# Kernel tuning notes

Hardware: AMD Instinct MI355X
Metric: run time of the kernel (lower is better)

## Reference

```python
import jax, jax.numpy as jnp
import numpy as np

B, T, D, H = 8, 512, 1024, 16
DH = D // H  # per-head feature dim (64)


def setup_inputs() -> dict:
    key = jax.random.key(0)
    ks = jax.random.split(key, 10)
    s = 1.0 / np.sqrt(DH)
    inp = {
        "X_data": jax.random.normal(ks[0], (B, T, D), dtype=jnp.float32),
        "mask": jnp.ones((B, T), dtype=jnp.int32),
        # per-head Q/K/V projections (each SelfAttention has its own d_h x d_h weights)
        "Wq": jax.random.normal(ks[1], (H, DH, DH), dtype=jnp.float32) * s,
        "bq": jnp.zeros((H, DH), dtype=jnp.float32),
        "Wk": jax.random.normal(ks[2], (H, DH, DH), dtype=jnp.float32) * s,
        "bk": jnp.zeros((H, DH), dtype=jnp.float32),
        "Wv": jax.random.normal(ks[3], (H, DH, DH), dtype=jnp.float32) * s,
        "bv": jnp.zeros((H, DH), dtype=jnp.float32),
        # AttentionFusion: linear on concatenated head outputs -> len_feature_new
        "Wf": jax.random.normal(ks[4], (D, D), dtype=jnp.float32) * (1.0 / np.sqrt(D)),
        "bf": jnp.zeros((D,), dtype=jnp.float32),
    }
    return inp


def reference(X_data, mask, Wq, bq, Wk, bk, Wv, bv, Wf, bf):
    # Split features into heads: [B, T, H, DH] (equal partitions since D % H == 0)
    Xh = X_data.reshape(B, T, H, DH)
    # Batched per-head projections (replaces the Python loop over heads)
    Q = jnp.einsum("bthd,hde->bhte", Xh, Wq) + bq[None, :, None, :]
    K = jnp.einsum("bthd,hde->bhte", Xh, Wk) + bk[None, :, None, :]
    V = jnp.einsum("bthd,hde->bhte", Xh, Wv) + bv[None, :, None, :]
    scale = 1.0 / jnp.sqrt(jnp.asarray(DH, dtype=Q.dtype))
    scores = jnp.einsum("bhqe,bhke->bhqk", Q, K) * scale  # [B, H, T, T]
    scores = jnp.where(mask[:, None, None, :] > 0, scores, jnp.asarray(-1e9, scores.dtype))
    att = jax.nn.softmax(scores, axis=-1)
    out = jnp.einsum("bhqk,bhke->bhqe", att, V)  # [B, H, T, DH]
    # Concatenate heads (same order as the per-head loop) and fuse
    out = out.transpose(0, 2, 1, 3).reshape(B, T, D)
    fused = out @ Wf + bf  # AttentionFusion linear
    return fused
```

## Files before the change

### kernel.cpp

```cpp
#include <hip/hip_runtime.h>
#include <math.h>

#define B 8
#define T 512
#define D 1024
#define H 16
#define DH 64

typedef __bf16 bf16;
typedef __attribute__((ext_vector_type(8))) __bf16 bf16x8;
typedef __attribute__((ext_vector_type(4))) __bf16 bf16x4;
typedef __attribute__((ext_vector_type(4))) float f32x4;

__device__ __forceinline__ void gld16(const void* g, void* l) {
    __builtin_amdgcn_global_load_lds(
        (const __attribute__((address_space(1))) void*)g,
        (__attribute__((address_space(3))) void*)l, 16, 0, 0);
}


__global__ __launch_bounds__(256) void wft_kernel(
    const float* __restrict__ Wf, bf16* __restrict__ WfT)
{
    __shared__ bf16 Ts[64 * 72];
    const int k0 = (blockIdx.x >> 4) * 64;
    const int n0 = (blockIdx.x & 15) * 64;
    const int tid = threadIdx.x;
    for (int i = tid; i < 1024; i += 256) {
        const int k = i >> 4, nq = (i & 15) * 4;
        const float4 w = *(const float4*)(Wf + (size_t)(k0 + k) * D + n0 + nq);
        Ts[(nq + 0) * 72 + k] = (bf16)w.x;
        Ts[(nq + 1) * 72 + k] = (bf16)w.y;
        Ts[(nq + 2) * 72 + k] = (bf16)w.z;
        Ts[(nq + 3) * 72 + k] = (bf16)w.w;
    }
    __syncthreads();
    for (int i = tid; i < 512; i += 256) {
        const int n = i >> 3, kc = (i & 7) * 8;
        *(bf16x8*)(WfT + (size_t)(n0 + n) * D + k0 + kc) = *(const bf16x8*)&Ts[n * 72 + kc];
    }
}

__global__ __launch_bounds__(256) void qkv_mfma(
    const float* __restrict__ X,
    const float* __restrict__ Wq, const float* __restrict__ bq,
    const float* __restrict__ Wk, const float* __restrict__ bk,
    const float* __restrict__ Wv, const float* __restrict__ bv,
    bf16* __restrict__ Qb, bf16* __restrict__ Kb, bf16* __restrict__ Vtb)
{
    __shared__ bf16 As[128 * 72];
    __shared__ bf16 Bq[64 * 72];
    __shared__ bf16 Bk[64 * 72];
    __shared__ bf16 Bv[64 * 72];
    __shared__ bf16 Vt_l[64 * 136];

    const int bh = blockIdx.x >> 2;
    const int t0 = (blockIdx.x & 3) * 128;
    const int b = bh >> 4, h = bh & 15;
    const int tid = threadIdx.x;
    const int wave = tid >> 6, lane = tid & 63;
    const int quad = lane >> 4, l15 = lane & 15;

    for (int i = tid; i < 2048; i += 256) {
        const int row = i >> 4, cq = (i & 15) * 4;
        const float4 x = *(const float4*)(X + ((size_t)b * T + t0 + row) * D + h * DH + cq);
        bf16x4 t;
        t[0] = (bf16)x.x; t[1] = (bf16)x.y; t[2] = (bf16)x.z; t[3] = (bf16)x.w;
        *(bf16x4*)&As[row * 72 + cq] = t;
    }
    for (int i = tid; i < 1024; i += 256) {
        const int d = i >> 4, eq = (i & 15) * 4;
        const float4 wq4 = *(const float4*)(Wq + h * 4096 + d * 64 + eq);
        const float4 wk4 = *(const float4*)(Wk + h * 4096 + d * 64 + eq);
        const float4 wv4 = *(const float4*)(Wv + h * 4096 + d * 64 + eq);
        Bq[(eq + 0) * 72 + d] = (bf16)wq4.x; Bq[(eq + 1) * 72 + d] = (bf16)wq4.y;
        Bq[(eq + 2) * 72 + d] = (bf16)wq4.z; Bq[(eq + 3) * 72 + d] = (bf16)wq4.w;
        Bk[(eq + 0) * 72 + d] = (bf16)wk4.x; Bk[(eq + 1) * 72 + d] = (bf16)wk4.y;
        Bk[(eq + 2) * 72 + d] = (bf16)wk4.z; Bk[(eq + 3) * 72 + d] = (bf16)wk4.w;
        Bv[(eq + 0) * 72 + d] = (bf16)wv4.x; Bv[(eq + 1) * 72 + d] = (bf16)wv4.y;
        Bv[(eq + 2) * 72 + d] = (bf16)wv4.z; Bv[(eq + 3) * 72 + d] = (bf16)wv4.w;
    }
    __syncthreads();

    bf16x8 af[2][2];
#pragma unroll
    for (int mt = 0; mt < 2; ++mt)
#pragma unroll
        for (int ks = 0; ks < 2; ++ks)
            af[mt][ks] = *(const bf16x8*)&As[(wave * 32 + mt * 16 + l15) * 72 + ks * 32 + quad * 8];

    auto compute = [&](const bf16* Bmat, f32x4 acc[2][4]) {
#pragma unroll
        for (int ks = 0; ks < 2; ++ks) {
            bf16x8 bfr[4];
#pragma unroll
            for (int nt = 0; nt < 4; ++nt)
                bfr[nt] = *(const bf16x8*)&Bmat[(nt * 16 + l15) * 72 + ks * 32 + quad * 8];
#pragma unroll
            for (int mt = 0; mt < 2; ++mt)
#pragma unroll
                for (int nt = 0; nt < 4; ++nt)
                    acc[mt][nt] = __builtin_amdgcn_mfma_f32_16x16x32_bf16(
                        af[mt][ks], bfr[nt], acc[mt][nt], 0, 0, 0);
        }
    };

    const size_t bhTD = (size_t)bh * T * DH;

    {
        f32x4 acc[2][4] = {};
        compute(Bq, acc);
#pragma unroll
        for (int mt = 0; mt < 2; ++mt)
#pragma unroll
            for (int nt = 0; nt < 4; ++nt) {
                const int e = nt * 16 + l15;
                const float bias = bq[h * DH + e];
#pragma unroll
                for (int reg = 0; reg < 4; ++reg) {
                    const int t = t0 + wave * 32 + mt * 16 + quad * 4 + reg;
                    Qb[bhTD + (size_t)t * DH + e] = (bf16)((acc[mt][nt][reg] + bias) * 0.125f);
                }
            }
    }
    {
        f32x4 acc[2][4] = {};
        compute(Bk, acc);
#pragma unroll
        for (int mt = 0; mt < 2; ++mt)
#pragma unroll
            for (int nt = 0; nt < 4; ++nt) {
                const int e = nt * 16 + l15;
                const float bias = bk[h * DH + e];
#pragma unroll
                for (int reg = 0; reg < 4; ++reg) {
                    const int t = t0 + wave * 32 + mt * 16 + quad * 4 + reg;
                    Kb[bhTD + (size_t)t * DH + e] = (bf16)(acc[mt][nt][reg] + bias);
                }
            }
    }
    {
        f32x4 acc[2][4] = {};
        compute(Bv, acc);
#pragma unroll
        for (int mt = 0; mt < 2; ++mt)
#pragma unroll
            for (int nt = 0; nt < 4; ++nt) {
                const int e = nt * 16 + l15;
                const float bias = bv[h * DH + e];
#pragma unroll
                for (int reg = 0; reg < 4; ++reg) {
                    const int tl = wave * 32 + mt * 16 + quad * 4 + reg;
                    Vt_l[e * 136 + tl] = (bf16)(acc[mt][nt][reg] + bias);
                }
            }
    }
    __syncthreads();
    for (int i = tid; i < 1024; i += 256) {
        const int e = i >> 4, c = (i & 15) * 8;
        const bf16x8 t = *(const bf16x8*)&Vt_l[e * 136 + c];
        *(bf16x8*)(Vtb + (size_t)bh * DH * T + (size_t)e * T + t0 + c) = t;
    }
}

__global__ __launch_bounds__(256) void attn_mfma(
    const bf16* __restrict__ Qb, const bf16* __restrict__ Kb,
    const bf16* __restrict__ Vtb, const int* __restrict__ mask,
    bf16* __restrict__ Ob)
{
    __shared__ bf16 Ks[64 * 64];
    __shared__ bf16 Vts[64 * 64];
    __shared__ bf16 Pl[4][32 * 72];
    __shared__ int ms[64];

    const int bh = blockIdx.x >> 2;
    const int q0 = (blockIdx.x & 3) * 128;
    const int b = bh >> 4, h = bh & 15;
    const int tid = threadIdx.x;
    const int wave = tid >> 6, lane = tid & 63;
    const int quad = lane >> 4, l15 = lane & 15;
    const int lrow = lane >> 3, lcol8 = (lane & 7) * 8;

    const size_t bhTD = (size_t)bh * T * DH;
    const size_t bhDT = (size_t)bh * DH * T;

    bf16x8 qf[2][2];
#pragma unroll
    for (int mt = 0; mt < 2; ++mt)
#pragma unroll
        for (int ks = 0; ks < 2; ++ks)
            qf[mt][ks] = *(const bf16x8*)(Qb + bhTD +
                (size_t)(q0 + wave * 32 + mt * 16 + l15) * DH + ks * 32 + quad * 8);

    f32x4 acc[2][4] = {};
    float lst[2][4] = {};

    for (int kt = 0; kt < 8; ++kt) {
        const int k0 = kt * 64;
        __syncthreads();
        {
            const int r0 = wave * 16;
            gld16(Kb + bhTD + (size_t)(k0 + r0 + lrow) * DH + lcol8, &Ks[r0 * 64]);
            gld16(Kb + bhTD + (size_t)(k0 + r0 + 8 + lrow) * DH + lcol8, &Ks[(r0 + 8) * 64]);
            gld16(Vtb + bhDT + (size_t)(r0 + lrow) * T + k0 + lcol8, &Vts[r0 * 64]);
            gld16(Vtb + bhDT + (size_t)(r0 + 8 + lrow) * T + k0 + lcol8, &Vts[(r0 + 8) * 64]);
            if (tid < 64) ms[tid] = mask[(size_t)b * T + k0 + tid];
        }
        __syncthreads();

        bf16x8 kf[4][2];
#pragma unroll
        for (int nt = 0; nt < 4; ++nt)
#pragma unroll
            for (int ks = 0; ks < 2; ++ks)
                kf[nt][ks] = *(const bf16x8*)&Ks[(nt * 16 + l15) * 64 + ks * 32 + quad * 8];
        int mv[4];
#pragma unroll
        for (int nt = 0; nt < 4; ++nt) mv[nt] = ms[nt * 16 + l15];

#pragma unroll
        for (int mt = 0; mt < 2; ++mt) {
            f32x4 s[4] = {};
#pragma unroll
            for (int ks = 0; ks < 2; ++ks)
#pragma unroll
                for (int nt = 0; nt < 4; ++nt)
                    s[nt] = __builtin_amdgcn_mfma_f32_16x16x32_bf16(qf[mt][ks], kf[nt][ks], s[nt], 0, 0, 0);
#pragma unroll
            for (int nt = 0; nt < 4; ++nt)
#pragma unroll
                for (int reg = 0; reg < 4; ++reg) {
                    const float p = (mv[nt] > 0) ? __expf(s[nt][reg]) : 0.f;
                    lst[mt][reg] += p;
                    Pl[wave][(mt * 16 + quad * 4 + reg) * 72 + nt * 16 + l15] = (bf16)p;
                }
        }
        __builtin_amdgcn_wave_barrier();

        bf16x8 vf[4][2];
#pragma unroll
        for (int nt = 0; nt < 4; ++nt)
#pragma unroll
            for (int kc = 0; kc < 2; ++kc)
                vf[nt][kc] = *(const bf16x8*)&Vts[(nt * 16 + l15) * 64 + kc * 32 + quad * 8];
#pragma unroll
        for (int mt = 0; mt < 2; ++mt) {
            bf16x8 pf[2];
#pragma unroll
            for (int kc = 0; kc < 2; ++kc)
                pf[kc] = *(const bf16x8*)&Pl[wave][(mt * 16 + l15) * 72 + kc * 32 + quad * 8];
#pragma unroll
            for (int nt = 0; nt < 4; ++nt)
#pragma unroll
                for (int kc = 0; kc < 2; ++kc)
                    acc[mt][nt] = __builtin_amdgcn_mfma_f32_16x16x32_bf16(pf[kc], vf[nt][kc], acc[mt][nt], 0, 0, 0);
        }
    }

#pragma unroll
    for (int mt = 0; mt < 2; ++mt)
#pragma unroll
        for (int reg = 0; reg < 4; ++reg) {
            float l = lst[mt][reg];
            l += __shfl_xor(l, 1);
            l += __shfl_xor(l, 2);
            l += __shfl_xor(l, 4);
            l += __shfl_xor(l, 8);
            const float inv = 1.f / l;
            const int t = q0 + wave * 32 + mt * 16 + quad * 4 + reg;
#pragma unroll
            for (int nt = 0; nt < 4; ++nt)
                Ob[((size_t)b * T + t) * D + h * DH + nt * 16 + l15] =
                    (bf16)(acc[mt][nt][reg] * inv);
        }
}

__global__ __launch_bounds__(256) void fuse_mfma(
    const bf16* __restrict__ Ob, const bf16* __restrict__ WfT,
    const float* __restrict__ bfv, float* __restrict__ out)
{
    __shared__ bf16 As[128 * 64];
    __shared__ bf16 Bs[128 * 64];

    const int col0 = blockIdx.x * 128;
    const int row0 = blockIdx.y * 128;
    const int tid = threadIdx.x;
    const int wave = tid >> 6, lane = tid & 63;
    const int quad = lane >> 4, l15 = lane & 15;
    const int lrow = lane >> 3, lcol8 = (lane & 7) * 8;
    const int wm = (wave >> 1) * 64, wn = (wave & 1) * 64;

    f32x4 acc[4][4] = {};

    for (int k0 = 0; k0 < D; k0 += 64) {
        __syncthreads();
        const int r0 = wave * 32;
#pragma unroll
        for (int j = 0; j < 4; ++j) {
            gld16(Ob + (size_t)(row0 + r0 + j * 8 + lrow) * D + k0 + lcol8, &As[(r0 + j * 8) * 64]);
            gld16(WfT + (size_t)(col0 + r0 + j * 8 + lrow) * D + k0 + lcol8, &Bs[(r0 + j * 8) * 64]);
        }
        __syncthreads();
#pragma unroll
        for (int ks = 0; ks < 2; ++ks) {
            bf16x8 af[4], bfr[4];
#pragma unroll
            for (int mt = 0; mt < 4; ++mt)
                af[mt] = *(const bf16x8*)&As[(wm + mt * 16 + l15) * 64 + ks * 32 + quad * 8];
#pragma unroll
            for (int nt = 0; nt < 4; ++nt)
                bfr[nt] = *(const bf16x8*)&Bs[(wn + nt * 16 + l15) * 64 + ks * 32 + quad * 8];
#pragma unroll
            for (int mt = 0; mt < 4; ++mt)
#pragma unroll
                for (int nt = 0; nt < 4; ++nt)
                    acc[mt][nt] = __builtin_amdgcn_mfma_f32_16x16x32_bf16(af[mt], bfr[nt], acc[mt][nt], 0, 0, 0);
        }
    }

    float bias[4];
#pragma unroll
    for (int nt = 0; nt < 4; ++nt) bias[nt] = bfv[col0 + wn + nt * 16 + l15];
#pragma unroll
    for (int mt = 0; mt < 4; ++mt)
#pragma unroll
        for (int reg = 0; reg < 4; ++reg) {
            const int r = row0 + wm + mt * 16 + quad * 4 + reg;
#pragma unroll
            for (int nt = 0; nt < 4; ++nt)
                out[(size_t)r * D + col0 + wn + nt * 16 + l15] = acc[mt][nt][reg] + bias[nt];
        }
}

extern "C" void kernel_launch(void* const* d_in, const int* in_sizes, int n_in,
                              void* d_out, int out_size, void* d_ws, size_t ws_size,
                              hipStream_t stream) {
    const float* X   = (const float*)d_in[0];
    const int* mask  = (const int*)d_in[1];
    const float* Wq  = (const float*)d_in[2];
    const float* bq  = (const float*)d_in[3];
    const float* Wk  = (const float*)d_in[4];
    const float* bk  = (const float*)d_in[5];
    const float* Wv  = (const float*)d_in[6];
    const float* bv  = (const float*)d_in[7];
    const float* Wf  = (const float*)d_in[8];
    const float* bfv = (const float*)d_in[9];
    float* out = (float*)d_out;

    bf16* wsb = (bf16*)d_ws;
    const size_t QN = (size_t)B * H * T * DH;
    bf16* Qb  = wsb;
    bf16* Kb  = wsb + QN;
    bf16* Vtb = wsb + 2 * QN;
    bf16* Ob  = wsb + 3 * QN;
    bf16* WfT = wsb + 4 * QN;

    wft_kernel<<<dim3(256), 256, 0, stream>>>(Wf, WfT);
    qkv_mfma<<<dim3(B * H * 4), 256, 0, stream>>>(X, Wq, bq, Wk, bk, Wv, bv, Qb, Kb, Vtb);
    attn_mfma<<<dim3(B * H * 4), 256, 0, stream>>>(Qb, Kb, Vtb, mask, Ob);
    fuse_mfma<<<dim3(D / 128, (B * T) / 128), 256, 0, stream>>>(Ob, WfT, bfv, out);
}
```

Baseline: 148.3 us.

## Add prep kernel for bf16 casts, XOR-swizzle LDS, enlarge attention key tiles, shrink fuse tiles

A single prep kernel now converts X to bf16 and transposes the per-head Wq/Wk/Wv and Wf weights into bf16, so qkv_mfma can stage its operands with global_load_lds and XOR-swizzled LDS layouts. Attention processes 128-key tiles instead of 64, halving the K/V loop iterations and barriers, and uses swizzled K/Vt tiles. The fuse GEMM drops to 128x64 tiles, doubling the block count for occupancy. In exchange it adds an extra pass over X through memory and uses more LDS in attention.

```diff
diff --git a/kernel.cpp b/kernel.cpp
--- a/kernel.cpp
+++ b/kernel.cpp
@@ -19,66 +19,88 @@
 }
 
 
-__global__ __launch_bounds__(256) void wft_kernel(
-    const float* __restrict__ Wf, bf16* __restrict__ WfT)
+__global__ __launch_bounds__(256) void prep_kernel(
+    const float* __restrict__ X,
+    const float* __restrict__ Wq, const float* __restrict__ Wk,
+    const float* __restrict__ Wv, const float* __restrict__ Wf,
+    bf16* __restrict__ Xb, bf16* __restrict__ WqT, bf16* __restrict__ WkT,
+    bf16* __restrict__ WvT, bf16* __restrict__ WfT)
 {
     __shared__ bf16 Ts[64 * 72];
-    const int k0 = (blockIdx.x >> 4) * 64;
-    const int n0 = (blockIdx.x & 15) * 64;
-    const int tid = threadIdx.x;
-    for (int i = tid; i < 1024; i += 256) {
-        const int k = i >> 4, nq = (i & 15) * 4;
-        const float4 w = *(const float4*)(Wf + (size_t)(k0 + k) * D + n0 + nq);
-        Ts[(nq + 0) * 72 + k] = (bf16)w.x;
-        Ts[(nq + 1) * 72 + k] = (bf16)w.y;
-        Ts[(nq + 2) * 72 + k] = (bf16)w.z;
-        Ts[(nq + 3) * 72 + k] = (bf16)w.w;
-    }
-    __syncthreads();
-    for (int i = tid; i < 512; i += 256) {
-        const int n = i >> 3, kc = (i & 7) * 8;
-        *(bf16x8*)(WfT + (size_t)(n0 + n) * D + k0 + kc) = *(const bf16x8*)&Ts[n * 72 + kc];
+    const int blk = blockIdx.x, tid = threadIdx.x;
+    if (blk < 256) {
+        const float4* src = (const float4*)X + (size_t)blk * 4096;
+        bf16x4* dst = (bf16x4*)Xb + (size_t)blk * 4096;
+#pragma unroll
+        for (int k = 0; k < 16; ++k) {
+            const float4 v = src[k * 256 + tid];
+            bf16x4 t;
+            t[0] = (bf16)v.x; t[1] = (bf16)v.y; t[2] = (bf16)v.z; t[3] = (bf16)v.w;
+            dst[k * 256 + tid] = t;
+        }
+    } else if (blk < 304) {
+        const int idx = blk - 256, m = idx >> 4, h = idx & 15;
+        const float* src = (m == 0 ? Wq : (m == 1 ? Wk : Wv)) + h * 4096;
+        bf16* dst = (m == 0 ? WqT : (m == 1 ? WkT : WvT)) + h * 4096;
+        for (int i = tid; i < 1024; i += 256) {
+            const int d = i >> 4, eq = (i & 15) * 4;
+            const float4 w = *(const float4*)(src + d * 64 + eq);
+            Ts[(eq + 0) * 72 + d] = (bf16)w.x; Ts[(eq + 1) * 72 + d] = (bf16)w.y;
+            Ts[(eq + 2) * 72 + d] = (bf16)w.z; Ts[(eq + 3) * 72 + d] = (bf16)w.w;
+        }
+        __syncthreads();
+        for (int i = tid; i < 512; i += 256) {
+            const int e = i >> 3, kc = (i & 7) * 8;
+            *(bf16x8*)(dst + e * 64 + kc) = *(const bf16x8*)&Ts[e * 72 + kc];
+        }
+    } else {
+        const int ti = blk - 304, k0 = (ti >> 4) * 64, n0 = (ti & 15) * 64;
+        for (int i = tid; i < 1024; i += 256) {
+            const int k = i >> 4, nq = (i & 15) * 4;
+            const float4 w = *(const float4*)(Wf + (size_t)(k0 + k) * D + n0 + nq);
+            Ts[(nq + 0) * 72 + k] = (bf16)w.x; Ts[(nq + 1) * 72 + k] = (bf16)w.y;
+            Ts[(nq + 2) * 72 + k] = (bf16)w.z; Ts[(nq + 3) * 72 + k] = (bf16)w.w;
+        }
+        __syncthreads();
+        for (int i = tid; i < 512; i += 256) {
+            const int n = i >> 3, kc = (i & 7) * 8;
+            *(bf16x8*)(WfT + (size_t)(n0 + n) * D + k0 + kc) = *(const bf16x8*)&Ts[n * 72 + kc];
+        }
     }
 }
 
 __global__ __launch_bounds__(256) void qkv_mfma(
-    const float* __restrict__ X,
-    const float* __restrict__ Wq, const float* __restrict__ bq,
-    const float* __restrict__ Wk, const float* __restrict__ bk,
-    const float* __restrict__ Wv, const float* __restrict__ bv,
+    const bf16* __restrict__ Xb,
+    const bf16* __restrict__ WqT, const bf16* __restrict__ WkT,
+    const bf16* __restrict__ WvT,
+    const float* __restrict__ bq, const float* __restrict__ bk,
+    const float* __restrict__ bv,
     bf16* __restrict__ Qb, bf16* __restrict__ Kb, bf16* __restrict__ Vtb)
 {
-    __shared__ bf16 As[128 * 72];
-    __shared__ bf16 Bq[64 * 72];
-    __shared__ bf16 Bk[64 * 72];
-    __shared__ bf16 Bv[64 * 72];
+    __shared__ bf16 Xs[128 * 64];
+    __shared__ bf16 Wqs[64 * 64], Wks[64 * 64], Wvs[64 * 64];
     __shared__ bf16 Vt_l[64 * 136];
 
-    const int bh = blockIdx.x >> 2;
-    const int t0 = (blockIdx.x & 3) * 128;
+    const int bh = blockIdx.x >> 2, t0 = (blockIdx.x & 3) * 128;
     const int b = bh >> 4, h = bh & 15;
-    const int tid = threadIdx.x;
-    const int wave = tid >> 6, lane = tid & 63;
+    const int tid = threadIdx.x, wave = tid >> 6, lane = tid & 63;
     const int quad = lane >> 4, l15 = lane & 15;
-
-    for (int i = tid; i < 2048; i += 256) {
-        const int row = i >> 4, cq = (i & 15) * 4;
-        const float4 x = *(const float4*)(X + ((size_t)b * T + t0 + row) * D + h * DH + cq);
-        bf16x4 t;
-        t[0] = (bf16)x.x; t[1] = (bf16)x.y; t[2] = (bf16)x.z; t[3] = (bf16)x.w;
-        *(bf16x4*)&As[row * 72 + cq] = t;
-    }
-    for (int i = tid; i < 1024; i += 256) {
-        const int d = i >> 4, eq = (i & 15) * 4;
-        const float4 wq4 = *(const float4*)(Wq + h * 4096 + d * 64 + eq);
-        const float4 wk4 = *(const float4*)(Wk + h * 4096 + d * 64 + eq);
-        const float4 wv4 = *(const float4*)(Wv + h * 4096 + d * 64 + eq);
-        Bq[(eq + 0) * 72 + d] = (bf16)wq4.x; Bq[(eq + 1) * 72 + d] = (bf16)wq4.y;
-        Bq[(eq + 2) * 72 + d] = (bf16)wq4.z; Bq[(eq + 3) * 72 + d] = (bf16)wq4.w;
-        Bk[(eq + 0) * 72 + d] = (bf16)wk4.x; Bk[(eq + 1) * 72 + d] = (bf16)wk4.y;
-        Bk[(eq + 2) * 72 + d] = (bf16)wk4.z; Bk[(eq + 3) * 72 + d] = (bf16)wk4.w;
-        Bv[(eq + 0) * 72 + d] = (bf16)wv4.x; Bv[(eq + 1) * 72 + d] = (bf16)wv4.y;
-        Bv[(eq + 2) * 72 + d] = (bf16)wv4.z; Bv[(eq + 3) * 72 + d] = (bf16)wv4.w;
+    const int lr = lane >> 3, lc = lane & 7;
+    const int csw = (lc ^ lr) * 8;
+
+    {
+        const int r0 = wave * 32;
+#pragma unroll
+        for (int j = 0; j < 4; ++j)
+            gld16(Xb + (size_t)(b * T + t0 + r0 + j * 8 + lr) * D + h * DH + csw,
+                  &Xs[(r0 + j * 8) * 64]);
+        const int r1 = wave * 16;
+#pragma unroll
+        for (int j = 0; j < 2; ++j) {
+            gld16(WqT + (size_t)h * 4096 + (r1 + j * 8 + lr) * 64 + csw, &Wqs[(r1 + j * 8) * 64]);
+            gld16(WkT + (size_t)h * 4096 + (r1 + j * 8 + lr) * 64 + csw, &Wks[(r1 + j * 8) * 64]);
+            gld16(WvT + (size_t)h * 4096 + (r1 + j * 8 + lr) * 64 + csw, &Wvs[(r1 + j * 8) * 64]);
+        }
     }
     __syncthreads();
 
@@ -86,8 +108,10 @@
 #pragma unroll
     for (int mt = 0; mt < 2; ++mt)
 #pragma unroll
-        for (int ks = 0; ks < 2; ++ks)
-            af[mt][ks] = *(const bf16x8*)&As[(wave * 32 + mt * 16 + l15) * 72 + ks * 32 + quad * 8];
+        for (int ks = 0; ks < 2; ++ks) {
+            const int row = wave * 32 + mt * 16 + l15;
+            af[mt][ks] = *(const bf16x8*)&Xs[row * 64 + ((ks * 4 + quad) ^ (l15 & 7)) * 8];
+        }
 
     auto compute = [&](const bf16* Bmat, f32x4 acc[2][4]) {
 #pragma unroll
@@ -95,7 +119,7 @@
             bf16x8 bfr[4];
 #pragma unroll
             for (int nt = 0; nt < 4; ++nt)
-                bfr[nt] = *(const bf16x8*)&Bmat[(nt * 16 + l15) * 72 + ks * 32 + quad * 8];
+                bfr[nt] = *(const bf16x8*)&Bmat[(nt * 16 + l15) * 64 + ((ks * 4 + quad) ^ (l15 & 7)) * 8];
 #pragma unroll
             for (int mt = 0; mt < 2; ++mt)
 #pragma unroll
@@ -109,7 +133,7 @@
 
     {
         f32x4 acc[2][4] = {};
-        compute(Bq, acc);
+        compute(Wqs, acc);
 #pragma unroll
         for (int mt = 0; mt < 2; ++mt)
 #pragma unroll
@@ -125,7 +149,7 @@
     }
     {
         f32x4 acc[2][4] = {};
-        compute(Bk, acc);
+        compute(Wks, acc);
 #pragma unroll
         for (int mt = 0; mt < 2; ++mt)
 #pragma unroll
@@ -141,7 +165,7 @@
     }
     {
         f32x4 acc[2][4] = {};
-        compute(Bv, acc);
+        compute(Wvs, acc);
 #pragma unroll
         for (int mt = 0; mt < 2; ++mt)
 #pragma unroll
@@ -168,18 +192,17 @@
     const bf16* __restrict__ Vtb, const int* __restrict__ mask,
     bf16* __restrict__ Ob)
 {
-    __shared__ bf16 Ks[64 * 64];
-    __shared__ bf16 Vts[64 * 64];
-    __shared__ bf16 Pl[4][32 * 72];
-    __shared__ int ms[64];
-
-    const int bh = blockIdx.x >> 2;
-    const int q0 = (blockIdx.x & 3) * 128;
+    __shared__ bf16 Ks[128 * 64];
+    __shared__ bf16 Vts[64 * 128];
+    __shared__ bf16 Pl[4][32 * 136];
+    __shared__ int msk[128];
+
+    const int bh = blockIdx.x >> 2, q0 = (blockIdx.x & 3) * 128;
     const int b = bh >> 4, h = bh & 15;
-    const int tid = threadIdx.x;
-    const int wave = tid >> 6, lane = tid & 63;
+    const int tid = threadIdx.x, wave = tid >> 6, lane = tid & 63;
     const int quad = lane >> 4, l15 = lane & 15;
-    const int lrow = lane >> 3, lcol8 = (lane & 7) * 8;
+    const int lr = lane >> 3, lc = lane & 7;
+    const int csw = (lc ^ lr) * 8;
 
     const size_t bhTD = (size_t)bh * T * DH;
     const size_t bhDT = (size_t)bh * DH * T;
@@ -195,65 +218,59 @@
     f32x4 acc[2][4] = {};
     float lst[2][4] = {};
 
-    for (int kt = 0; kt < 8; ++kt) {
-        const int k0 = kt * 64;
+    for (int kt = 0; kt < 4; ++kt) {
+        const int k0 = kt * 128;
         __syncthreads();
         {
-            const int r0 = wave * 16;
-            gld16(Kb + bhTD + (size_t)(k0 + r0 + lrow) * DH + lcol8, &Ks[r0 * 64]);
-            gld16(Kb + bhTD + (size_t)(k0 + r0 + 8 + lrow) * DH + lcol8, &Ks[(r0 + 8) * 64]);
-            gld16(Vtb + bhDT + (size_t)(r0 + lrow) * T + k0 + lcol8, &Vts[r0 * 64]);
-            gld16(Vtb + bhDT + (size_t)(r0 + 8 + lrow) * T + k0 + lcol8, &Vts[(r0 + 8) * 64]);
-            if (tid < 64) ms[tid] = mask[(size_t)b * T + k0 + tid];
-        }
-        __syncthreads();
-
-        bf16x8 kf[4][2];
-#pragma unroll
-        for (int nt = 0; nt < 4; ++nt)
-#pragma unroll
-            for (int ks = 0; ks < 2; ++ks)
-                kf[nt][ks] = *(const bf16x8*)&Ks[(nt * 16 + l15) * 64 + ks * 32 + quad * 8];
-        int mv[4];
-#pragma unroll
-        for (int nt = 0; nt < 4; ++nt) mv[nt] = ms[nt * 16 + l15];
-
-#pragma unroll
-        for (int mt = 0; mt < 2; ++mt) {
-            f32x4 s[4] = {};
-#pragma unroll
-            for (int ks = 0; ks < 2; ++ks)
-#pragma unroll
-                for (int nt = 0; nt < 4; ++nt)
-                    s[nt] = __builtin_amdgcn_mfma_f32_16x16x32_bf16(qf[mt][ks], kf[nt][ks], s[nt], 0, 0, 0);
-#pragma unroll
-            for (int nt = 0; nt < 4; ++nt)
+            const int r0 = wave * 32;
+#pragma unroll
+            for (int j = 0; j < 4; ++j)
+                gld16(Kb + bhTD + (size_t)(k0 + r0 + j * 8 + lr) * DH + csw,
+                      &Ks[(r0 + j * 8) * 64]);
+            const int e0 = wave * 16;
+#pragma unroll
+            for (int j = 0; j < 4; ++j) {
+                const int er = j * 4 + (lane >> 4);
+                const int csw2 = ((lane & 15) ^ er) * 8;
+                gld16(Vtb + bhDT + (size_t)(e0 + er) * T + k0 + csw2,
+                      &Vts[(e0 + j * 4) * 128]);
+            }
+            if (tid < 128) msk[tid] = mask[(size_t)b * T + k0 + tid];
+        }
+        __syncthreads();
+
+#pragma unroll
+        for (int nt = 0; nt < 8; ++nt) {
+            const int krow = nt * 16 + l15;
+            const bf16x8 kf0 = *(const bf16x8*)&Ks[krow * 64 + ((quad) ^ (l15 & 7)) * 8];
+            const bf16x8 kf1 = *(const bf16x8*)&Ks[krow * 64 + ((4 + quad) ^ (l15 & 7)) * 8];
+            const int mv = msk[krow];
+#pragma unroll
+            for (int mt = 0; mt < 2; ++mt) {
+                f32x4 s = {};
+                s = __builtin_amdgcn_mfma_f32_16x16x32_bf16(qf[mt][0], kf0, s, 0, 0, 0);
+                s = __builtin_amdgcn_mfma_f32_16x16x32_bf16(qf[mt][1], kf1, s, 0, 0, 0);
 #pragma unroll
                 for (int reg = 0; reg < 4; ++reg) {
-                    const float p = (mv[nt] > 0) ? __expf(s[nt][reg]) : 0.f;
+                    const float p = (mv > 0) ? __expf(s[reg]) : 0.f;
                     lst[mt][reg] += p;
-                    Pl[wave][(mt * 16 + quad * 4 + reg) * 72 + nt * 16 + l15] = (bf16)p;
+                    Pl[wave][(mt * 16 + quad * 4 + reg) * 136 + nt * 16 + l15] = (bf16)p;
                 }
+            }
         }
         __builtin_amdgcn_wave_barrier();
 
-        bf16x8 vf[4][2];
-#pragma unroll
-        for (int nt = 0; nt < 4; ++nt)
-#pragma unroll
-            for (int kc = 0; kc < 2; ++kc)
-                vf[nt][kc] = *(const bf16x8*)&Vts[(nt * 16 + l15) * 64 + kc * 32 + quad * 8];
-#pragma unroll
-        for (int mt = 0; mt < 2; ++mt) {
-            bf16x8 pf[2];
-#pragma unroll
-            for (int kc = 0; kc < 2; ++kc)
-                pf[kc] = *(const bf16x8*)&Pl[wave][(mt * 16 + l15) * 72 + kc * 32 + quad * 8];
-#pragma unroll
-            for (int nt = 0; nt < 4; ++nt)
-#pragma unroll
-                for (int kc = 0; kc < 2; ++kc)
-                    acc[mt][nt] = __builtin_amdgcn_mfma_f32_16x16x32_bf16(pf[kc], vf[nt][kc], acc[mt][nt], 0, 0, 0);
+#pragma unroll
+        for (int kc = 0; kc < 4; ++kc) {
+            const bf16x8 pf0 = *(const bf16x8*)&Pl[wave][(l15) * 136 + kc * 32 + quad * 8];
+            const bf16x8 pf1 = *(const bf16x8*)&Pl[wave][(16 + l15) * 136 + kc * 32 + quad * 8];
+#pragma unroll
+            for (int nt = 0; nt < 4; ++nt) {
+                const int erow = nt * 16 + l15;
+                const bf16x8 vf = *(const bf16x8*)&Vts[erow * 128 + ((kc * 4 + quad) ^ (l15 & 15)) * 8];
+                acc[0][nt] = __builtin_amdgcn_mfma_f32_16x16x32_bf16(pf0, vf, acc[0][nt], 0, 0, 0);
+                acc[1][nt] = __builtin_amdgcn_mfma_f32_16x16x32_bf16(pf1, vf, acc[1][nt], 0, 0, 0);
+            }
         }
     }
 
@@ -280,38 +297,41 @@
     const float* __restrict__ bfv, float* __restrict__ out)
 {
     __shared__ bf16 As[128 * 64];
-    __shared__ bf16 Bs[128 * 64];
-
-    const int col0 = blockIdx.x * 128;
+    __shared__ bf16 Bs[64 * 64];
+
+    const int col0 = blockIdx.x * 64;
     const int row0 = blockIdx.y * 128;
-    const int tid = threadIdx.x;
-    const int wave = tid >> 6, lane = tid & 63;
+    const int tid = threadIdx.x, wave = tid >> 6, lane = tid & 63;
     const int quad = lane >> 4, l15 = lane & 15;
-    const int lrow = lane >> 3, lcol8 = (lane & 7) * 8;
-    const int wm = (wave >> 1) * 64, wn = (wave & 1) * 64;
-
-    f32x4 acc[4][4] = {};
+    const int lr = lane >> 3, lc = lane & 7;
+    const int csw = (lc ^ lr) * 8;
+    const int wm = wave * 32;
+
+    f32x4 acc[2][4] = {};
 
     for (int k0 = 0; k0 < D; k0 += 64) {
         __syncthreads();
-        const int r0 = wave * 32;
-#pragma unroll
-        for (int j = 0; j < 4; ++j) {
-            gld16(Ob + (size_t)(row0 + r0 + j * 8 + lrow) * D + k0 + lcol8, &As[(r0 + j * 8) * 64]);
-            gld16(WfT + (size_t)(col0 + r0 + j * 8 + lrow) * D + k0 + lcol8, &Bs[(r0 + j * 8) * 64]);
-        }
+#pragma unroll
+        for (int j = 0; j < 4; ++j)
+            gld16(Ob + (size_t)(row0 + wm + j * 8 + lr) * D + k0 + csw, &As[(wm + j * 8) * 64]);
+#pragma unroll
+        for (int j = 0; j < 2; ++j)
+            gld16(WfT + (size_t)(col0 + wave * 16 + j * 8 + lr) * D + k0 + csw,
+                  &Bs[(wave * 16 + j * 8) * 64]);
         __syncthreads();
 #pragma unroll
         for (int ks = 0; ks < 2; ++ks) {
-            bf16x8 af[4], bfr[4];
-#pragma unroll
-            for (int mt = 0; mt < 4; ++mt)
-                af[mt] = *(const bf16x8*)&As[(wm + mt * 16 + l15) * 64 + ks * 32 + quad * 8];
+            bf16x8 af[2], bfr[4];
+#pragma unroll
+            for (int mt = 0; mt < 2; ++mt) {
+                const int row = wm + mt * 16 + l15;
+                af[mt] = *(const bf16x8*)&As[row * 64 + ((ks * 4 + quad) ^ (l15 & 7)) * 8];
+            }
 #pragma unroll
             for (int nt = 0; nt < 4; ++nt)
-                bfr[nt] = *(const bf16x8*)&Bs[(wn + nt * 16 + l15) * 64 + ks * 32 + quad * 8];
-#pragma unroll
-            for (int mt = 0; mt < 4; ++mt)
+                bfr[nt] = *(const bf16x8*)&Bs[(nt * 16 + l15) * 64 + ((ks * 4 + quad) ^ (l15 & 7)) * 8];
+#pragma unroll
+            for (int mt = 0; mt < 2; ++mt)
 #pragma unroll
                 for (int nt = 0; nt < 4; ++nt)
                     acc[mt][nt] = __builtin_amdgcn_mfma_f32_16x16x32_bf16(af[mt], bfr[nt], acc[mt][nt], 0, 0, 0);
@@ -320,15 +340,15 @@
 
     float bias[4];
 #pragma unroll
-    for (int nt = 0; nt < 4; ++nt) bias[nt] = bfv[col0 + wn + nt * 16 + l15];
-#pragma unroll
-    for (int mt = 0; mt < 4; ++mt)
+    for (int nt = 0; nt < 4; ++nt) bias[nt] = bfv[col0 + nt * 16 + l15];
+#pragma unroll
+    for (int mt = 0; mt < 2; ++mt)
 #pragma unroll
         for (int reg = 0; reg < 4; ++reg) {
             const int r = row0 + wm + mt * 16 + quad * 4 + reg;
 #pragma unroll
             for (int nt = 0; nt < 4; ++nt)
-                out[(size_t)r * D + col0 + wn + nt * 16 + l15] = acc[mt][nt][reg] + bias[nt];
+                out[(size_t)r * D + col0 + nt * 16 + l15] = acc[mt][nt][reg] + bias[nt];
         }
 }
 
@@ -354,9 +374,13 @@
     bf16* Vtb = wsb + 2 * QN;
     bf16* Ob  = wsb + 3 * QN;
     bf16* WfT = wsb + 4 * QN;
-
-    wft_kernel<<<dim3(256), 256, 0, stream>>>(Wf, WfT);
-    qkv_mfma<<<dim3(B * H * 4), 256, 0, stream>>>(X, Wq, bq, Wk, bk, Wv, bv, Qb, Kb, Vtb);
+    bf16* WqT = WfT + (size_t)D * D;
+    bf16* WkT = WqT + H * DH * DH;
+    bf16* WvT = WkT + H * DH * DH;
+    bf16* Xb  = WvT + H * DH * DH;
+
+    prep_kernel<<<dim3(560), 256, 0, stream>>>(X, Wq, Wk, Wv, Wf, Xb, WqT, WkT, WvT, WfT);
+    qkv_mfma<<<dim3(B * H * 4), 256, 0, stream>>>(Xb, WqT, WkT, WvT, bq, bk, bv, Qb, Kb, Vtb);
     attn_mfma<<<dim3(B * H * 4), 256, 0, stream>>>(Qb, Kb, Vtb, mask, Ob);
-    fuse_mfma<<<dim3(D / 128, (B * T) / 128), 256, 0, stream>>>(Ob, WfT, bfv, out);
-}
+    fuse_mfma<<<dim3(D / 64, (B * T) / 128), 256, 0, stream>>>(Ob, WfT, bfv, out);
+}
```

New measurement: 133.6 us. 9.9% less time.
